# Kernel tuning notes

Hardware: AMD Instinct MI355X
Metric: run time of the kernel (lower is better)

## Reference

```python
import jax, jax.numpy as jnp
import numpy as np

# ---- pywt filter banks (dec_lo, dec_hi, rec_lo, rec_hi), all pywt-ordered ----
_SQ2 = 0.7071067811865476

def _orth(dec_lo):
    dec_lo = np.asarray(dec_lo, dtype=np.float64)
    rec_lo = dec_lo[::-1].copy()
    k = np.arange(len(dec_lo))
    dec_hi = ((-1.0) ** (k + 1)) * rec_lo
    rec_hi = dec_hi[::-1].copy()
    return dec_lo, dec_hi, rec_lo, rec_hi

_DB4 = [-0.010597401784997278, 0.032883011666982945, 0.030841381835986965,
        -0.18703481171888114, -0.02798376941698385, 0.6308807679295904,
        0.7148465705525415, 0.23037781330885523]
_SYM6 = [-0.007800708325034148, 0.0017677118642428036, 0.04472490177066578,
         -0.021060292512300564, -0.07263752278646252, 0.3379294217276218,
         0.787641141030194, 0.4910559419267466, -0.048311742585633,
         -0.11799011114819057, 0.0034907120842174702, 0.015404109327027373]
_BIOR13 = (
    np.array([-0.08838834764831845, 0.08838834764831845, _SQ2, _SQ2, 0.08838834764831845, -0.08838834764831845]),
    np.array([0.0, 0.0, -_SQ2, _SQ2, 0.0, 0.0]),
    np.array([0.0, 0.0, _SQ2, _SQ2, 0.0, 0.0]),
    np.array([-0.08838834764831845, -0.08838834764831845, _SQ2, -_SQ2, 0.08838834764831845, 0.08838834764831845]),
)

WAVELETS = ['haar', 'db4', 'sym6', 'bior1.3']
FILTERS = {
    'haar': _orth([_SQ2, _SQ2]),
    'db4': _orth(_DB4),
    'sym6': _orth(_SYM6),
    'bior1.3': _BIOR13,
}
FILTERS = {k: tuple(jnp.asarray(f, dtype=jnp.float32) for f in v) for k, v in FILTERS.items()}


def _dwt(x, dec_lo, dec_hi):
    # x: [B, C, T] (T even). ptwt: reflect-pad (2L-3)//2 each side, stride-2 corr with flipped dec filters.
    B, C, T = x.shape
    L = dec_lo.shape[0]
    p = (2 * L - 3) // 2
    xp = jnp.pad(x, ((0, 0), (0, 0), (p, p)), mode='reflect') if p > 0 else x
    filt = jnp.stack([dec_lo[::-1], dec_hi[::-1]])[:, None, :].astype(x.dtype)  # [2,1,L]
    out = jax.lax.conv_general_dilated(
        xp.reshape(B * C, 1, -1), filt, window_strides=(2,), padding='VALID',
        dimension_numbers=('NCH', 'OIH', 'NCH'))
    out = out.reshape(B, C, 2, -1)
    return out[:, :, 0], out[:, :, 1]  # approx, detail: [B, C, (T+L-2)//2]


def _idwt(lo, hi, rec_lo, rec_hi):
    # conv_transpose stride 2 with rec filters, then crop (2L-3)//2 per side (ptwt waverec).
    B, C, Tc = lo.shape
    L = rec_lo.shape[0]
    p = (2 * L - 3) // 2
    c = jnp.stack([lo, hi], axis=2).reshape(B * C, 2, Tc)
    filt = jnp.stack([rec_lo[::-1], rec_hi[::-1]])[None].astype(lo.dtype)  # [1,2,L]
    y = jax.lax.conv_general_dilated(
        c, filt, window_strides=(1,), padding=[(L - 1, L - 1)],
        lhs_dilation=(2,), dimension_numbers=('NCH', 'OIH', 'NCH'))
    y = y.reshape(B, C, -1)
    if p > 0:
        y = y[:, :, p:-p]
    return y


def _spectral(z, lam, gamma, cos_theta):
    return gamma * jnp.sign(z) * jax.nn.relu(jnp.abs(z) - lam) * cos_theta


def setup_inputs() -> dict:
    key = jax.random.key(0)
    ks = jax.random.split(key, 8)
    B, S, E = 8, 4096, 1024
    x = jax.random.normal(ks[0], (B, S, E), dtype=jnp.float32)
    lambda_approx = jnp.full((1, E, 1), 0.05, jnp.float32) + 0.01 * jax.random.uniform(ks[1], (1, E, 1), jnp.float32)
    lambda_detail = jnp.full((1, E, 1), 0.05, jnp.float32) + 0.01 * jax.random.uniform(ks[2], (1, E, 1), jnp.float32)
    log_gamma = 0.1 * jax.random.normal(ks[3], (1, E, 1), jnp.float32)
    theta = 0.1 * jax.random.normal(ks[4], (1, E, 1), jnp.float32)
    basis_logits = 0.5 * jax.random.normal(ks[5], (4,), jnp.float32)
    ln_weight = jnp.ones((E,), jnp.float32)
    ln_bias = jnp.zeros((E,), jnp.float32)
    return {'x': x, 'lambda_approx': lambda_approx, 'lambda_detail': lambda_detail,
            'log_gamma': log_gamma, 'theta': theta, 'basis_logits': basis_logits,
            'ln_weight': ln_weight, 'ln_bias': ln_bias}


def reference(x, lambda_approx, lambda_detail, log_gamma, theta, basis_logits, ln_weight, ln_bias):
    residual = x                       # [B, S, E]
    S = x.shape[1]
    xt = jnp.transpose(x, (0, 2, 1))   # [B, E, S]
    gamma = jax.nn.softplus(log_gamma) + 1e-6
    ct = jnp.cos(theta)
    weights = jax.nn.softmax(basis_logits)  # all 4 wavelets valid for even S
    out = jnp.zeros_like(xt)
    for i, name in enumerate(WAVELETS):
        dl, dh, rl, rh = FILTERS[name]
        lo, hi = _dwt(xt, dl, dh)
        lo = _spectral(lo, lambda_approx, gamma, ct)
        hi = _spectral(hi, lambda_detail, gamma, ct)
        rec = _idwt(lo, hi, rl, rh)[:, :, :S]
        out = out + weights[i] * rec
    y = jnp.transpose(out, (0, 2, 1)) + residual
    mu = jnp.mean(y, axis=-1, keepdims=True)
    var = jnp.var(y, axis=-1, keepdims=True)
    return (y - mu) / jnp.sqrt(var + 1e-5) * ln_weight + ln_bias
```

## Files before the change

### kernel.cpp

```cpp
#include <hip/hip_runtime.h>
#include <cstdint>

#define T_SEQ 4096
#define E_DIM 1024
#define N_B   8
#define SC    128
#define TILE_P 148
#define LDS_ST 149

constexpr int LW[4] = {2, 8, 12, 6};

constexpr float DLf[4][12] = {
  {0.7071067811865476f, 0.7071067811865476f, 0,0,0,0,0,0,0,0,0,0},
  {-0.010597401784997278f, 0.032883011666982945f, 0.030841381835986965f, -0.18703481171888114f,
   -0.02798376941698385f, 0.6308807679295904f, 0.7148465705525415f, 0.23037781330885523f, 0,0,0,0},
  {-0.007800708325034148f, 0.0017677118642428036f, 0.04472490177066578f, -0.021060292512300564f,
   -0.07263752278646252f, 0.3379294217276218f, 0.787641141030194f, 0.4910559419267466f,
   -0.048311742585633f, -0.11799011114819057f, 0.0034907120842174702f, 0.015404109327027373f},
  {-0.08838834764831845f, 0.08838834764831845f, 0.7071067811865476f, 0.7071067811865476f,
    0.08838834764831845f, -0.08838834764831845f, 0,0,0,0,0,0},
};
constexpr float DHf[4][12] = {
  {-0.7071067811865476f, 0.7071067811865476f, 0,0,0,0,0,0,0,0,0,0},
  {-0.23037781330885523f, 0.7148465705525415f, -0.6308807679295904f, -0.02798376941698385f,
    0.18703481171888114f, 0.030841381835986965f, -0.032883011666982945f, -0.010597401784997278f, 0,0,0,0},
  {-0.015404109327027373f, 0.0034907120842174702f, 0.11799011114819057f, -0.048311742585633f,
   -0.4910559419267466f, 0.787641141030194f, -0.3379294217276218f, -0.07263752278646252f,
    0.021060292512300564f, 0.04472490177066578f, -0.0017677118642428036f, -0.007800708325034148f},
  {0,0,-0.7071067811865476f, 0.7071067811865476f, 0,0, 0,0,0,0,0,0},
};
constexpr float RLf[4][12] = {
  {0.7071067811865476f, 0.7071067811865476f, 0,0,0,0,0,0,0,0,0,0},
  {0.23037781330885523f, 0.7148465705525415f, 0.6308807679295904f, -0.02798376941698385f,
   -0.18703481171888114f, 0.030841381835986965f, 0.032883011666982945f, -0.010597401784997278f, 0,0,0,0},
  {0.015404109327027373f, 0.0034907120842174702f, -0.11799011114819057f, -0.048311742585633f,
   0.4910559419267466f, 0.787641141030194f, 0.3379294217276218f, -0.07263752278646252f,
   -0.021060292512300564f, 0.04472490177066578f, 0.0017677118642428036f, -0.007800708325034148f},
  {0,0,0.7071067811865476f, 0.7071067811865476f, 0,0, 0,0,0,0,0,0},
};
constexpr float RHf[4][12] = {
  {0.7071067811865476f, -0.7071067811865476f, 0,0,0,0,0,0,0,0,0,0},
  {-0.010597401784997278f, -0.032883011666982945f, 0.030841381835986965f, 0.18703481171888114f,
   -0.02798376941698385f, -0.6308807679295904f, 0.7148465705525415f, -0.23037781330885523f, 0,0,0,0},
  {-0.007800708325034148f, -0.0017677118642428036f, 0.04472490177066578f, 0.021060292512300564f,
   -0.07263752278646252f, -0.3379294217276218f, 0.787641141030194f, -0.4910559419267466f,
   -0.048311742585633f, 0.11799011114819057f, 0.0034907120842174702f, -0.015404109327027373f},
  {-0.08838834764831845f, -0.08838834764831845f, 0.7071067811865476f, -0.7071067811865476f,
    0.08838834764831845f, 0.08838834764831845f, 0,0,0,0,0,0},
};

template <int W>
__device__ __forceinline__ void wavelet_accum(const float (&xw)[52], float (&acc)[32],
                                              float la, float ld, float g2, float wgt) {
  constexpr int L  = LW[W];
  constexpr int KT = L / 2 + 15;
#pragma unroll
  for (int kk = 0; kk < KT; ++kk) {
    float lo = 0.f, hi = 0.f;
#pragma unroll
    for (int m = 0; m < L; ++m) {
      const float xv = xw[2 * kk + 11 - m];
      if (DLf[W][m] != 0.0f) lo = fmaf(DLf[W][m], xv, lo);
      if (DHf[W][m] != 0.0f) hi = fmaf(DHf[W][m], xv, hi);
    }
    const float loS = g2 * copysignf(fmaxf(fabsf(lo) - la, 0.f), lo);
    const float hiS = g2 * copysignf(fmaxf(fabsf(hi) - ld, 0.f), hi);
#pragma unroll
    for (int m = 0; m < L; ++m) {
      const int j = 2 * kk + m + 2 - L;
      if (j >= 0 && j < 32) {
        float c = 0.f;
        if (RLf[W][m] != 0.0f) c = fmaf(loS, RLf[W][m], c);
        if (RHf[W][m] != 0.0f) c = fmaf(hiS, RHf[W][m], c);
        acc[j] = fmaf(wgt, c, acc[j]);
      }
    }
  }
}

__global__ __launch_bounds__(256, 3) void wlm_k1(
    const float* __restrict__ x,
    const float* __restrict__ la_, const float* __restrict__ ld_,
    const float* __restrict__ lg_, const float* __restrict__ th_,
    const float* __restrict__ bl_, float* __restrict__ y) {
  __shared__ float xs[64][LDS_ST];

  const int tid  = threadIdx.x;
  const int lane = tid & 63;
  const int wave = tid >> 6;
  const int s0 = blockIdx.x * SC;
  const int e0 = blockIdx.y * 64;
  const int b  = blockIdx.z;

  {
    const int ch4 = (tid & 15) * 4;
#pragma unroll
    for (int it = 0; it < 10; ++it) {
      const int pos = (tid >> 4) + it * 16;
      if (pos < TILE_P) {
        int g = s0 - 10 + pos;
        g = (g < 0) ? -g : g;
        g = (g >= T_SEQ) ? (2 * T_SEQ - 2 - g) : g;
        const float4 v = *reinterpret_cast<const float4*>(
            &x[((size_t)b * T_SEQ + g) * E_DIM + e0 + ch4]);
        xs[ch4 + 0][pos] = v.x;
        xs[ch4 + 1][pos] = v.y;
        xs[ch4 + 2][pos] = v.z;
        xs[ch4 + 3][pos] = v.w;
      }
    }
  }

  const int e = e0 + lane;
  const float la = la_[e];
  const float ld = ld_[e];
  const float lg = lg_[e];
  const float th = th_[e];
  const float sp = fmaxf(lg, 0.f) + log1pf(expf(-fabsf(lg)));
  const float g2 = (sp + 1e-6f) * cosf(th);

  const float b0 = bl_[0], b1 = bl_[1], b2 = bl_[2], b3 = bl_[3];
  const float mx = fmaxf(fmaxf(b0, b1), fmaxf(b2, b3));
  float w0 = expf(b0 - mx), w1 = expf(b1 - mx), w2 = expf(b2 - mx), w3 = expf(b3 - mx);
  const float wsum = w0 + w1 + w2 + w3;
  w0 /= wsum; w1 /= wsum; w2 /= wsum; w3 /= wsum;

  __syncthreads();

  float xw[52];
#pragma unroll
  for (int i = 0; i < 52; ++i) xw[i] = xs[lane][wave * 32 + i];
#pragma unroll
  for (int i = 0; i < 52; ++i) asm volatile("" : "+v"(xw[i]));

  float acc[32];
#pragma unroll
  for (int j = 0; j < 32; ++j) acc[j] = 0.f;

  wavelet_accum<0>(xw, acc, la, ld, g2, w0);
  wavelet_accum<1>(xw, acc, la, ld, g2, w1);
  wavelet_accum<2>(xw, acc, la, ld, g2, w2);
  wavelet_accum<3>(xw, acc, la, ld, g2, w3);

  const int sA = s0 + wave * 32;
#pragma unroll
  for (int j = 0; j < 32; ++j) {
    y[((size_t)b * T_SEQ + sA + j) * E_DIM + e] = xw[j + 10] + acc[j];
  }
}

__global__ __launch_bounds__(256) void wlm_k2(float* __restrict__ y,
                                              const float* __restrict__ w,
                                              const float* __restrict__ bias) {
  const int token = blockIdx.x;
  const int tid = threadIdx.x;
  float* row = y + (size_t)token * E_DIM;

  float4 v = *reinterpret_cast<const float4*>(&row[tid * 4]);
  float s  = v.x + v.y + v.z + v.w;
  float sq = v.x * v.x + v.y * v.y + v.z * v.z + v.w * v.w;
#pragma unroll
  for (int off = 32; off; off >>= 1) {
    s  += __shfl_down(s, off);
    sq += __shfl_down(sq, off);
  }
  __shared__ float ps[4], pq[4], stat[2];
  const int wave = tid >> 6, lane = tid & 63;
  if (lane == 0) { ps[wave] = s; pq[wave] = sq; }
  __syncthreads();
  if (tid == 0) {
    const float S1 = ps[0] + ps[1] + ps[2] + ps[3];
    const float S2 = pq[0] + pq[1] + pq[2] + pq[3];
    const float mu = S1 * (1.f / E_DIM);
    const float var = S2 * (1.f / E_DIM) - mu * mu;
    stat[0] = mu;
    stat[1] = rsqrtf(var + 1e-5f);
  }
  __syncthreads();
  const float mu = stat[0], rstd = stat[1];
  const float4 wv = *reinterpret_cast<const float4*>(&w[tid * 4]);
  const float4 bv = *reinterpret_cast<const float4*>(&bias[tid * 4]);
  float4 o;
  o.x = (v.x - mu) * rstd * wv.x + bv.x;
  o.y = (v.y - mu) * rstd * wv.y + bv.y;
  o.z = (v.z - mu) * rstd * wv.z + bv.z;
  o.w = (v.w - mu) * rstd * wv.w + bv.w;
  *reinterpret_cast<float4*>(&row[tid * 4]) = o;
}

extern "C" void kernel_launch(void* const* d_in, const int* in_sizes, int n_in,
                              void* d_out, int out_size, void* d_ws, size_t ws_size,
                              hipStream_t stream) {
  const float* x   = (const float*)d_in[0];
  const float* la  = (const float*)d_in[1];
  const float* ldt = (const float*)d_in[2];
  const float* lg  = (const float*)d_in[3];
  const float* th  = (const float*)d_in[4];
  const float* bl  = (const float*)d_in[5];
  const float* lnw = (const float*)d_in[6];
  const float* lnb = (const float*)d_in[7];
  float* out = (float*)d_out;

  dim3 g1(T_SEQ / SC, E_DIM / 64, N_B);
  wlm_k1<<<g1, 256, 0, stream>>>(x, la, ldt, lg, th, bl, out);
  wlm_k2<<<dim3(N_B * T_SEQ), 256, 0, stream>>>(out, lnw, lnb);
}
```

Before: 114.2 us.

## Pack two channels per thread with float2 math and reshape wavelet tiles

Each thread now handles two channels (e and e+64) as a float2 vector, so the compiler can emit packed FP32 instructions (v_pk_fma) on the wavelet filter math. Each block covers 128 channels and 64 time steps, and the LDS layout becomes position-major with float4 stores. Soft-thresholding is rewritten with fmed3, and the softmax weight is folded into the gain to save multiplies. The cost is a larger relative halo (84 loaded rows for 64 outputs) and more redundant filter work at tile edges per output.

New measurement: 114.1 us. About the same (-0.1%).

```diff
diff --git a/kernel.cpp b/kernel.cpp
--- a/kernel.cpp
+++ b/kernel.cpp
@@ -4,9 +4,9 @@
 #define T_SEQ 4096
 #define E_DIM 1024
 #define N_B   8
-#define SC    128
-#define TILE_P 148
-#define LDS_ST 149
+#define SC    64
+#define TILE_P 84
+typedef float v2f __attribute__((ext_vector_type(2)));
 
 constexpr int LW[4] = {2, 8, 12, 6};
 
@@ -49,30 +49,35 @@
     0.08838834764831845f, 0.08838834764831845f, 0,0,0,0,0,0},
 };
 
+__device__ __forceinline__ v2f sv(float c) { return v2f{c, c}; }
+
 template <int W>
-__device__ __forceinline__ void wavelet_accum(const float (&xw)[52], float (&acc)[32],
-                                              float la, float ld, float g2, float wgt) {
+__device__ __forceinline__ void wavelet_accum(const v2f (&xw)[36], v2f (&acc)[16],
+                                              v2f la, v2f ld, v2f gw) {
   constexpr int L  = LW[W];
-  constexpr int KT = L / 2 + 15;
+  constexpr int KT = L / 2 + 7;
 #pragma unroll
   for (int kk = 0; kk < KT; ++kk) {
-    float lo = 0.f, hi = 0.f;
+    v2f lo = {0.f, 0.f}, hi = {0.f, 0.f};
 #pragma unroll
     for (int m = 0; m < L; ++m) {
-      const float xv = xw[2 * kk + 11 - m];
-      if (DLf[W][m] != 0.0f) lo = fmaf(DLf[W][m], xv, lo);
-      if (DHf[W][m] != 0.0f) hi = fmaf(DHf[W][m], xv, hi);
+      const v2f xv = xw[2 * kk + 11 - m];
+      if (DLf[W][m] != 0.0f) lo += sv(DLf[W][m]) * xv;
+      if (DHf[W][m] != 0.0f) hi += sv(DHf[W][m]) * xv;
     }
-    const float loS = g2 * copysignf(fmaxf(fabsf(lo) - la, 0.f), lo);
-    const float hiS = g2 * copysignf(fmaxf(fabsf(hi) - ld, 0.f), hi);
+    v2f cl, ch;
+    cl.x = __builtin_amdgcn_fmed3f(lo.x, -la.x, la.x);
+    cl.y = __builtin_amdgcn_fmed3f(lo.y, -la.y, la.y);
+    ch.x = __builtin_amdgcn_fmed3f(hi.x, -ld.x, ld.x);
+    ch.y = __builtin_amdgcn_fmed3f(hi.y, -ld.y, ld.y);
+    const v2f loS = (lo - cl) * gw;
+    const v2f hiS = (hi - ch) * gw;
 #pragma unroll
     for (int m = 0; m < L; ++m) {
       const int j = 2 * kk + m + 2 - L;
-      if (j >= 0 && j < 32) {
-        float c = 0.f;
-        if (RLf[W][m] != 0.0f) c = fmaf(loS, RLf[W][m], c);
-        if (RHf[W][m] != 0.0f) c = fmaf(hiS, RHf[W][m], c);
-        acc[j] = fmaf(wgt, c, acc[j]);
+      if (j >= 0 && j < 16) {
+        if (RLf[W][m] != 0.0f) acc[j] += loS * sv(RLf[W][m]);
+        if (RHf[W][m] != 0.0f) acc[j] += hiS * sv(RHf[W][m]);
       }
     }
   }
@@ -83,69 +88,76 @@
     const float* __restrict__ la_, const float* __restrict__ ld_,
     const float* __restrict__ lg_, const float* __restrict__ th_,
     const float* __restrict__ bl_, float* __restrict__ y) {
-  __shared__ float xs[64][LDS_ST];
+  __shared__ float xs[TILE_P][2][64];
 
   const int tid  = threadIdx.x;
   const int lane = tid & 63;
   const int wave = tid >> 6;
   const int s0 = blockIdx.x * SC;
-  const int e0 = blockIdx.y * 64;
+  const int e0 = blockIdx.y * 128;
   const int b  = blockIdx.z;
 
   {
-    const int ch4 = (tid & 15) * 4;
-#pragma unroll
-    for (int it = 0; it < 10; ++it) {
-      const int pos = (tid >> 4) + it * 16;
+    const int c4  = (tid & 31) * 4;
+    const int sel = c4 >> 6;
+    const int cc  = c4 & 63;
+    const int prow = tid >> 5;
+#pragma unroll
+    for (int it = 0; it < 11; ++it) {
+      const int pos = prow + it * 8;
       if (pos < TILE_P) {
         int g = s0 - 10 + pos;
         g = (g < 0) ? -g : g;
         g = (g >= T_SEQ) ? (2 * T_SEQ - 2 - g) : g;
         const float4 v = *reinterpret_cast<const float4*>(
-            &x[((size_t)b * T_SEQ + g) * E_DIM + e0 + ch4]);
-        xs[ch4 + 0][pos] = v.x;
-        xs[ch4 + 1][pos] = v.y;
-        xs[ch4 + 2][pos] = v.z;
-        xs[ch4 + 3][pos] = v.w;
+            &x[((size_t)b * T_SEQ + g) * E_DIM + e0 + c4]);
+        *reinterpret_cast<float4*>(&xs[pos][sel][cc]) = v;
       }
     }
   }
 
-  const int e = e0 + lane;
-  const float la = la_[e];
-  const float ld = ld_[e];
-  const float lg = lg_[e];
-  const float th = th_[e];
-  const float sp = fmaxf(lg, 0.f) + log1pf(expf(-fabsf(lg)));
-  const float g2 = (sp + 1e-6f) * cosf(th);
+  const int e = e0 + lane, e2 = e + 64;
+  const v2f la = {la_[e], la_[e2]};
+  const v2f ld = {ld_[e], ld_[e2]};
+  const v2f lg = {lg_[e], lg_[e2]};
+  const v2f th = {th_[e], th_[e2]};
+  v2f g2;
+  g2.x = (fmaxf(lg.x, 0.f) + log1pf(expf(-fabsf(lg.x))) + 1e-6f) * cosf(th.x);
+  g2.y = (fmaxf(lg.y, 0.f) + log1pf(expf(-fabsf(lg.y))) + 1e-6f) * cosf(th.y);
 
   const float b0 = bl_[0], b1 = bl_[1], b2 = bl_[2], b3 = bl_[3];
   const float mx = fmaxf(fmaxf(b0, b1), fmaxf(b2, b3));
-  float w0 = expf(b0 - mx), w1 = expf(b1 - mx), w2 = expf(b2 - mx), w3 = expf(b3 - mx);
-  const float wsum = w0 + w1 + w2 + w3;
-  w0 /= wsum; w1 /= wsum; w2 /= wsum; w3 /= wsum;
+  const float w0 = expf(b0 - mx), w1 = expf(b1 - mx),
+              w2 = expf(b2 - mx), w3 = expf(b3 - mx);
+  const float wr = 1.f / (w0 + w1 + w2 + w3);
+  const v2f gw0 = g2 * sv(w0 * wr), gw1 = g2 * sv(w1 * wr),
+            gw2 = g2 * sv(w2 * wr), gw3 = g2 * sv(w3 * wr);
 
   __syncthreads();
 
-  float xw[52];
-#pragma unroll
-  for (int i = 0; i < 52; ++i) xw[i] = xs[lane][wave * 32 + i];
-#pragma unroll
-  for (int i = 0; i < 52; ++i) asm volatile("" : "+v"(xw[i]));
-
-  float acc[32];
-#pragma unroll
-  for (int j = 0; j < 32; ++j) acc[j] = 0.f;
-
-  wavelet_accum<0>(xw, acc, la, ld, g2, w0);
-  wavelet_accum<1>(xw, acc, la, ld, g2, w1);
-  wavelet_accum<2>(xw, acc, la, ld, g2, w2);
-  wavelet_accum<3>(xw, acc, la, ld, g2, w3);
-
-  const int sA = s0 + wave * 32;
-#pragma unroll
-  for (int j = 0; j < 32; ++j) {
-    y[((size_t)b * T_SEQ + sA + j) * E_DIM + e] = xw[j + 10] + acc[j];
+  const int base = wave * 16;
+  v2f xw[36];
+#pragma unroll
+  for (int i = 0; i < 36; ++i) {
+    xw[i] = v2f{xs[base + i][0][lane], xs[base + i][1][lane]};
+  }
+
+  v2f acc[16];
+#pragma unroll
+  for (int j = 0; j < 16; ++j) acc[j] = v2f{0.f, 0.f};
+
+  wavelet_accum<0>(xw, acc, la, ld, gw0);
+  wavelet_accum<1>(xw, acc, la, ld, gw1);
+  wavelet_accum<2>(xw, acc, la, ld, gw2);
+  wavelet_accum<3>(xw, acc, la, ld, gw3);
+
+  const int sA = s0 + wave * 16;
+#pragma unroll
+  for (int j = 0; j < 16; ++j) {
+    const v2f o = xw[j + 10] + acc[j];
+    const size_t off = ((size_t)b * T_SEQ + sA + j) * E_DIM + e;
+    y[off]      = o.x;
+    y[off + 64] = o.y;
   }
 }
 
@@ -201,7 +213,7 @@
   const float* lnb = (const float*)d_in[7];
   float* out = (float*)d_out;
 
-  dim3 g1(T_SEQ / SC, E_DIM / 64, N_B);
+  dim3 g1(T_SEQ / SC, E_DIM / 128, N_B);
   wlm_k1<<<g1, 256, 0, stream>>>(x, la, ldt, lg, th, bl, out);
   wlm_k2<<<dim3(N_B * T_SEQ), 256, 0, stream>>>(out, lnw, lnb);
 }
```
